# Optimization experiments

Hardware: AMD Instinct MI355X
Metric: run time of the kernel (lower is better)

Reference implementation:

```python
import jax, jax.numpy as jnp
import numpy as np

N = 20000      # nodes
E = 320000     # edges (before self-loops)
F_IN = 512     # input feature size
HID = 128      # encoder hidden
OUT = 128      # encoder output / GAT in_channels
H = 4          # gat heads
C = 64         # gat out_channels per head


def setup_inputs() -> dict:
    key = jax.random.key(0)
    ks = jax.random.split(key, 10)
    s = 0.05
    return {
        "x": jax.random.normal(ks[0], (N, F_IN), jnp.float32),
        "edge_index": jax.random.randint(ks[1], (2, E), 0, N, dtype=jnp.int64),
        "W1": jax.random.normal(ks[2], (F_IN, HID), jnp.float32) * s,
        "b1": jax.random.normal(ks[3], (HID,), jnp.float32) * s,
        "W2": jax.random.normal(ks[4], (HID, OUT), jnp.float32) * s,
        "b2": jax.random.normal(ks[5], (OUT,), jnp.float32) * s,
        "Wg": jax.random.normal(ks[6], (OUT, H * C), jnp.float32) * s,
        "att_src": jax.random.normal(ks[7], (H, C), jnp.float32) * s,
        "att_dst": jax.random.normal(ks[8], (H, C), jnp.float32) * s,
        "bias_g": jax.random.normal(ks[9], (H * C,), jnp.float32) * s,
    }


def reference(x, edge_index, W1, b1, W2, b2, Wg, att_src, att_dst, bias_g):
    # MLP encoder: Linear -> ReLU -> Linear
    h = jnp.maximum(x @ W1 + b1, 0.0) @ W2 + b2            # [N, OUT]

    # GATConv (concat=True, eval mode -> no dropout)
    xg = (h @ Wg).reshape(N, H, C)                          # per-head projections

    # add self-loops (PyG GATConv default)
    loops = jnp.arange(N, dtype=edge_index.dtype)
    src = jnp.concatenate([edge_index[0], loops])           # [E+N] source j
    dst = jnp.concatenate([edge_index[1], loops])           # [E+N] dest   i

    a_src = jnp.einsum('nhc,hc->nh', xg, att_src)           # [N, H]
    a_dst = jnp.einsum('nhc,hc->nh', xg, att_dst)           # [N, H]

    e = jax.nn.leaky_relu(a_src[src] + a_dst[dst], 0.2)     # [E+N, H]

    # segment softmax over incoming edges of each destination node
    m = jax.ops.segment_max(e, dst, num_segments=N)         # [N, H]
    ex = jnp.exp(e - m[dst])
    denom = jax.ops.segment_sum(ex, dst, num_segments=N)
    alpha = ex / (denom[dst] + 1e-16)                       # [E+N, H]

    # weighted scatter-add aggregation
    out = jax.ops.segment_sum(alpha[:, :, None] * xg[src], dst, num_segments=N)  # [N, H, C]
    return out.reshape(N, H * C) + bias_g
```

## Files before the change

### kernel.cpp

```cpp
#include <hip/hip_runtime.h>
#include <math.h>

#define NNODES 20000
#define NEDGES 320000
#define FIN    512
#define HIDD   128
#define OUTD   128
#define NH     4
#define NC     64
#define HC     256

typedef short bf16x8 __attribute__((ext_vector_type(8)));
typedef float f32x4  __attribute__((ext_vector_type(4)));

__device__ __forceinline__ unsigned short f2bf(float f) {
    unsigned int u = __float_as_uint(f);
    unsigned int r = 0x7fffu + ((u >> 16) & 1u);
    return (unsigned short)((u + r) >> 16);
}
__device__ __forceinline__ float b2f(short t) {
    return __uint_as_float(((unsigned)(unsigned short)t) << 16);
}
__device__ __forceinline__ float4 f4max(float4 a, float4 b) {
    return make_float4(fmaxf(a.x,b.x), fmaxf(a.y,b.y), fmaxf(a.z,b.z), fmaxf(a.w,b.w));
}
__device__ __forceinline__ float4 f4add(float4 a, float4 b) {
    return make_float4(a.x+b.x, a.y+b.y, a.z+b.z, a.w+b.w);
}
__device__ __forceinline__ float4 f4sub(float4 a, float4 b) {
    return make_float4(a.x-b.x, a.y-b.y, a.z-b.z, a.w-b.w);
}
__device__ __forceinline__ float4 f4mul(float4 a, float4 b) {
    return make_float4(a.x*b.x, a.y*b.y, a.z*b.z, a.w*b.w);
}
__device__ __forceinline__ float4 f4exp(float4 a) {
    return make_float4(__expf(a.x), __expf(a.y), __expf(a.z), __expf(a.w));
}
__device__ __forceinline__ float4 shflx4(float4 v, int m) {
    return make_float4(__shfl_xor(v.x,m), __shfl_xor(v.y,m), __shfl_xor(v.z,m), __shfl_xor(v.w,m));
}

__global__ __launch_bounds__(256)
void transpose_cast_kernel(const float* __restrict__ W, unsigned short* __restrict__ Wt,
                           int K, int N) {
    int idx = blockIdx.x * 256 + threadIdx.x;
    if (idx >= K * N) return;
    int n = idx / K, k = idx % K;
    Wt[idx] = f2bf(W[(size_t)k * N + n]);
}

__global__ __launch_bounds__(256)
void fuse_w2g_kernel(const float* __restrict__ W2, const float* __restrict__ b2,
                     const float* __restrict__ Wg, unsigned short* __restrict__ W2gt,
                     float* __restrict__ b2g) {
    int idx = blockIdx.x * 256 + threadIdx.x;
    if (idx >= HC * HIDD) return;
    int n = idx >> 7;
    int k = idx & 127;
    float s = 0.f;
    #pragma unroll 8
    for (int t = 0; t < HIDD; ++t)
        s += W2[(size_t)k * OUTD + t] * Wg[(size_t)t * HC + n];
    W2gt[(size_t)n * HIDD + k] = f2bf(s);
    if (k == 0) {
        float t2 = 0.f;
        #pragma unroll 8
        for (int t = 0; t < OUTD; ++t) t2 += b2[t] * Wg[(size_t)t * HC + n];
        b2g[n] = t2;
    }
}

template<bool A_IS_F32, bool OUT_BF16>
__global__ __launch_bounds__(256)
void mfma_gemm_kernel(const void* __restrict__ Aptr,
                      const unsigned short* __restrict__ Bt,
                      const float* __restrict__ bias,
                      void* __restrict__ Cptr,
                      int M, int N, int K, int do_relu) {
    __shared__ unsigned short As[64 * 64];
    __shared__ unsigned short Bs[128 * 64];

    const int tid  = threadIdx.x;
    const int lane = tid & 63;
    const int w    = tid >> 6;
    const int wr   = w >> 1;
    const int wc   = w & 1;
    const int m0   = blockIdx.x * 64;
    const int n0   = blockIdx.y * 128;

    char* pA = (char*)As;
    char* pB = (char*)Bs;

    f32x4 acc[2][4];
    #pragma unroll
    for (int m = 0; m < 2; ++m)
        #pragma unroll
        for (int n = 0; n < 4; ++n) acc[m][n] = (f32x4){0.f, 0.f, 0.f, 0.f};

    for (int k0 = 0; k0 < K; k0 += 64) {
        if (A_IS_F32) {
            const int row = tid >> 2;
            const int ks  = (tid & 3) << 4;
            const bool ok = (m0 + row) < M;
            const float4* Ap = (const float4*)((const float*)Aptr +
                               (size_t)(m0 + row) * K + k0 + ks);
            float4 f0 = make_float4(0,0,0,0), f1 = f0, f2 = f0, f3 = f0;
            if (ok) { f0 = Ap[0]; f1 = Ap[1]; f2 = Ap[2]; f3 = Ap[3]; }
            unsigned short u[16];
            u[0]=f2bf(f0.x); u[1]=f2bf(f0.y); u[2]=f2bf(f0.z); u[3]=f2bf(f0.w);
            u[4]=f2bf(f1.x); u[5]=f2bf(f1.y); u[6]=f2bf(f1.z); u[7]=f2bf(f1.w);
            u[8]=f2bf(f2.x); u[9]=f2bf(f2.y); u[10]=f2bf(f2.z); u[11]=f2bf(f2.w);
            u[12]=f2bf(f3.x); u[13]=f2bf(f3.y); u[14]=f2bf(f3.z); u[15]=f2bf(f3.w);
            const int sw = (row & 7) << 4;
            const int base = row * 128 + ks * 2;
            *(bf16x8*)(pA + ((base     ) ^ sw)) = *(bf16x8*)&u[0];
            *(bf16x8*)(pA + ((base + 16) ^ sw)) = *(bf16x8*)&u[8];
        } else {
            const unsigned short* Ab = (const unsigned short*)Aptr;
            #pragma unroll
            for (int i = 0; i < 2; ++i) {
                int s   = tid + i * 256;
                int row = s >> 3;
                int sg  = s & 7;
                bf16x8 v = {};
                if ((m0 + row) < M)
                    v = *(const bf16x8*)(Ab + (size_t)(m0 + row) * K + k0 + sg * 8);
                *(bf16x8*)(pA + (((row * 128 + sg * 16)) ^ ((row & 7) << 4))) = v;
            }
        }
        #pragma unroll
        for (int i = 0; i < 4; ++i) {
            int s   = tid + i * 256;
            int col = s >> 3;
            int sg  = s & 7;
            bf16x8 v = *(const bf16x8*)(Bt + (size_t)(n0 + col) * K + k0 + sg * 8);
            *(bf16x8*)(pB + (((col * 128 + sg * 16)) ^ ((col & 7) << 4))) = v;
        }
        __syncthreads();

        #pragma unroll
        for (int ks = 0; ks < 2; ++ks) {
            const int kb = ks * 64 + ((lane >> 4) << 4);
            bf16x8 a[2], b[4];
            #pragma unroll
            for (int m = 0; m < 2; ++m) {
                int row = wr * 32 + m * 16 + (lane & 15);
                a[m] = *(const bf16x8*)(pA + ((row * 128 + kb) ^ ((row & 7) << 4)));
            }
            #pragma unroll
            for (int n = 0; n < 4; ++n) {
                int col = wc * 64 + n * 16 + (lane & 15);
                b[n] = *(const bf16x8*)(pB + ((col * 128 + kb) ^ ((col & 7) << 4)));
            }
            #pragma unroll
            for (int m = 0; m < 2; ++m)
                #pragma unroll
                for (int n = 0; n < 4; ++n)
                    acc[m][n] = __builtin_amdgcn_mfma_f32_16x16x32_bf16(
                        a[m], b[n], acc[m][n], 0, 0, 0);
        }
        __syncthreads();
    }

    #pragma unroll
    for (int n = 0; n < 4; ++n) {
        const int col = n0 + wc * 64 + n * 16 + (lane & 15);
        const float bv = bias ? bias[col] : 0.f;
        #pragma unroll
        for (int m = 0; m < 2; ++m) {
            #pragma unroll
            for (int r = 0; r < 4; ++r) {
                const int row = m0 + wr * 32 + m * 16 + ((lane >> 4) << 2) + r;
                if (row >= M) continue;
                float v = acc[m][n][r] + bv;
                if (do_relu) v = fmaxf(v, 0.f);
                if (OUT_BF16)
                    ((unsigned short*)Cptr)[(size_t)row * N + col] = f2bf(v);
                else
                    ((float*)Cptr)[(size_t)row * N + col] = v;
            }
        }
    }
}

__global__ __launch_bounds__(256)
void att_dots_kernel(const unsigned short* __restrict__ xgb, const float* __restrict__ att_src,
                     const float* __restrict__ att_dst, float* __restrict__ a_src,
                     float* __restrict__ a_dst, int n) {
    int idx = blockIdx.x * 256 + threadIdx.x;
    if (idx >= n * NH) return;
    int node = idx >> 2;
    int h = idx & 3;
    const bf16x8* xr = (const bf16x8*)(xgb + (size_t)node * HC + h * NC);
    const float* sa = att_src + h * NC;
    const float* da = att_dst + h * NC;
    float ss = 0.f, dd = 0.f;
    #pragma unroll
    for (int j = 0; j < 8; ++j) {
        bf16x8 v = xr[j];
        #pragma unroll
        for (int t = 0; t < 8; ++t) {
            float f = b2f(v[t]);
            ss += f * sa[j * 8 + t];
            dd += f * da[j * 8 + t];
        }
    }
    a_src[idx] = ss;
    a_dst[idx] = dd;
}

__global__ void init_deg_kernel(int* __restrict__ deg, int n) {
    int i = blockIdx.x * 256 + threadIdx.x;
    if (i < n) deg[i] = 1;
}

__global__ void count_deg_kernel(const int* __restrict__ dst, int* __restrict__ deg, int e) {
    int i = blockIdx.x * 256 + threadIdx.x;
    if (i < e) atomicAdd(&deg[dst[i]], 1);
}

__global__ __launch_bounds__(1024)
void scan_offsets_kernel(const int* __restrict__ deg, int* __restrict__ offs,
                         int* __restrict__ cursor, int n) {
    __shared__ int wsum[16], wbase[16];
    const int tid = threadIdx.x, lane = tid & 63, w = tid >> 6;
    const int i0 = tid * 20;
    int loc[20];
    int s = 0;
    #pragma unroll
    for (int k = 0; k < 20; ++k) {
        int i = i0 + k;
        int v = (i < n) ? deg[i] : 0;
        loc[k] = s;
        s += v;
    }
    int incl = s;
    #pragma unroll
    for (int d = 1; d < 64; d <<= 1) {
        int t = __shfl_up(incl, d);
        if (lane >= d) incl += t;
    }
    if (lane == 63) wsum[w] = incl;
    __syncthreads();
    if (w == 0) {
        int v = (lane < 16) ? wsum[lane] : 0;
        int sc = v;
        #pragma unroll
        for (int d = 1; d < 16; d <<= 1) {
            int t = __shfl_up(sc, d);
            if (lane >= d) sc += t;
        }
        if (lane < 16) wbase[lane] = sc - v;
    }
    __syncthreads();
    const int excl = wbase[w] + incl - s;
    #pragma unroll
    for (int k = 0; k < 20; ++k) {
        int i = i0 + k;
        if (i < n) { int o = excl + loc[k]; offs[i] = o; cursor[i] = o; }
    }
    if (tid == 1023) offs[n] = excl + s;
}

__global__ void scatter_e_kernel(const int* __restrict__ src, const int* __restrict__ dst,
                                 const float4* __restrict__ asrc, const float4* __restrict__ adst,
                                 int* __restrict__ cursor, int* __restrict__ csr_src,
                                 float4* __restrict__ e_csr, int e, int n) {
    int i = blockIdx.x * 256 + threadIdx.x;
    int s, d;
    if (i < e)          { s = src[i]; d = dst[i]; }
    else if (i < e + n) { s = i - e;  d = i - e;  }
    else return;
    float4 a = asrc[s], b = adst[d];
    float4 ev = make_float4(a.x + b.x, a.y + b.y, a.z + b.z, a.w + b.w);
    ev.x = ev.x > 0.f ? ev.x : 0.2f * ev.x;
    ev.y = ev.y > 0.f ? ev.y : 0.2f * ev.y;
    ev.z = ev.z > 0.f ? ev.z : 0.2f * ev.z;
    ev.w = ev.w > 0.f ? ev.w : 0.2f * ev.w;
    int slot = atomicAdd(&cursor[d], 1);
    csr_src[slot] = s;
    e_csr[slot] = ev;
}

__global__ __launch_bounds__(256)
void gat_aggregate2_kernel(const unsigned short* __restrict__ xgb,
                           const float4* __restrict__ e_csr,
                           const int* __restrict__ offs, const int* __restrict__ csr_src,
                           const float* __restrict__ bias, float* __restrict__ out, int n) {
    __shared__ float4 exbuf[4][64];
    __shared__ int    sbuf[4][64];
    const int wv   = threadIdx.x >> 6;
    const int lane = threadIdx.x & 63;
    const int node = blockIdx.x * 4 + wv;
    if (node >= n) return;
    const int beg = offs[node], end = offs[node + 1];
    const int deg = end - beg;

    float4 m   = make_float4(-INFINITY, -INFINITY, -INFINITY, -INFINITY);
    float4 den = make_float4(0.f, 0.f, 0.f, 0.f);
    for (int c0 = 0; c0 < deg; c0 += 64) {
        int idx = beg + c0 + lane;
        bool ok = idx < end;
        float4 e = ok ? e_csr[idx]
                      : make_float4(-INFINITY, -INFINITY, -INFINITY, -INFINITY);
        int s = ok ? csr_src[idx] : 0;
        float4 cm = e;
        #pragma unroll
        for (int dd = 32; dd >= 1; dd >>= 1) cm = f4max(cm, shflx4(cm, dd));
        float4 nm = f4max(m, cm);
        float4 ex = f4exp(f4sub(e, nm));
        exbuf[wv][lane] = ex;
        sbuf[wv][lane]  = s;
        float4 cs = ex;
        #pragma unroll
        for (int dd = 32; dd >= 1; dd >>= 1) cs = f4add(cs, shflx4(cs, dd));
        den = f4add(f4mul(den, f4exp(f4sub(m, nm))), cs);
        m = nm;
    }

    const int hi = lane >> 5;
    const int ll = lane & 31;
    const int h  = ll >> 3;
    const float denh = (h == 0) ? den.x : (h == 1) ? den.y : (h == 2) ? den.z : den.w;
    const float inv = 1.f / (denh + 1e-16f);

    float4 acc0 = make_float4(0.f, 0.f, 0.f, 0.f);
    float4 acc1 = make_float4(0.f, 0.f, 0.f, 0.f);
    const float* exf = (const float*)&exbuf[wv][0];

    auto run_chunk = [&](int cn) {
        int j = 0;
        for (; j + 4 <= cn; j += 4) {
            int jA = j + hi, jB = j + 2 + hi;
            int sA = sbuf[wv][jA], sB = sbuf[wv][jB];
            float wA = exf[jA * 4 + h], wB = exf[jB * 4 + h];
            bf16x8 vA = *(const bf16x8*)(xgb + (size_t)sA * HC + ll * 8);
            bf16x8 vB = *(const bf16x8*)(xgb + (size_t)sB * HC + ll * 8);
            acc0.x += wA * b2f(vA[0]); acc0.y += wA * b2f(vA[1]);
            acc0.z += wA * b2f(vA[2]); acc0.w += wA * b2f(vA[3]);
            acc1.x += wA * b2f(vA[4]); acc1.y += wA * b2f(vA[5]);
            acc1.z += wA * b2f(vA[6]); acc1.w += wA * b2f(vA[7]);
            acc0.x += wB * b2f(vB[0]); acc0.y += wB * b2f(vB[1]);
            acc0.z += wB * b2f(vB[2]); acc0.w += wB * b2f(vB[3]);
            acc1.x += wB * b2f(vB[4]); acc1.y += wB * b2f(vB[5]);
            acc1.z += wB * b2f(vB[6]); acc1.w += wB * b2f(vB[7]);
        }
        for (; j < cn; j += 2) {
            int jj = j + hi;
            bool ok2 = jj < cn;
            int s = sbuf[wv][ok2 ? jj : 0];
            float wgt = ok2 ? exf[jj * 4 + h] : 0.f;
            bf16x8 v = *(const bf16x8*)(xgb + (size_t)s * HC + ll * 8);
            acc0.x += wgt * b2f(v[0]); acc0.y += wgt * b2f(v[1]);
            acc0.z += wgt * b2f(v[2]); acc0.w += wgt * b2f(v[3]);
            acc1.x += wgt * b2f(v[4]); acc1.y += wgt * b2f(v[5]);
            acc1.z += wgt * b2f(v[6]); acc1.w += wgt * b2f(v[7]);
        }
    };

    if (deg <= 64) {
        run_chunk(deg);
    } else {
        for (int c0 = 0; c0 < deg; c0 += 64) {
            int idx = beg + c0 + lane;
            if (idx < end) {
                float4 e = e_csr[idx];
                exbuf[wv][lane] = f4exp(f4sub(e, m));
                sbuf[wv][lane]  = csr_src[idx];
            }
            int cn = deg - c0; if (cn > 64) cn = 64;
            run_chunk(cn);
        }
    }

    acc0.x += __shfl_xor(acc0.x, 32); acc0.y += __shfl_xor(acc0.y, 32);
    acc0.z += __shfl_xor(acc0.z, 32); acc0.w += __shfl_xor(acc0.w, 32);
    acc1.x += __shfl_xor(acc1.x, 32); acc1.y += __shfl_xor(acc1.y, 32);
    acc1.z += __shfl_xor(acc1.z, 32); acc1.w += __shfl_xor(acc1.w, 32);

    if (hi == 0) {
        const float4* b4 = (const float4*)bias;
        float4 bv0 = b4[ll * 2], bv1 = b4[ll * 2 + 1];
        float4 o0 = make_float4(acc0.x * inv + bv0.x, acc0.y * inv + bv0.y,
                                acc0.z * inv + bv0.z, acc0.w * inv + bv0.w);
        float4 o1 = make_float4(acc1.x * inv + bv1.x, acc1.y * inv + bv1.y,
                                acc1.z * inv + bv1.z, acc1.w * inv + bv1.w);
        float4* op = (float4*)(out + (size_t)node * HC) + ll * 2;
        op[0] = o0;
        op[1] = o1;
    }
}

extern "C" void kernel_launch(void* const* d_in, const int* in_sizes, int n_in,
                              void* d_out, int out_size, void* d_ws, size_t ws_size,
                              hipStream_t stream) {
    const float* x       = (const float*)d_in[0];
    const int*   ei      = (const int*)d_in[1];
    const float* W1      = (const float*)d_in[2];
    const float* b1      = (const float*)d_in[3];
    const float* W2      = (const float*)d_in[4];
    const float* b2      = (const float*)d_in[5];
    const float* Wg      = (const float*)d_in[6];
    const float* att_src = (const float*)d_in[7];
    const float* att_dst = (const float*)d_in[8];
    const float* bias_g  = (const float*)d_in[9];

    const int Nn = in_sizes[0] / FIN;
    const int E  = in_sizes[1] / 2;
    const int* e_src = ei;
    const int* e_dst = ei + E;

    char* w = (char*)d_ws;
    auto alloc = [&](size_t bytes) { char* p = w; w += (bytes + 255) & ~(size_t)255; return p; };
    unsigned short* W1t  = (unsigned short*)alloc((size_t)OUTD * FIN * 2);
    unsigned short* W2gt = (unsigned short*)alloc((size_t)HC * HIDD * 2);
    float* b2g  = (float*)alloc(HC * 4);
    unsigned short* h1  = (unsigned short*)alloc((size_t)Nn * HIDD * 2);
    unsigned short* xgb = (unsigned short*)alloc((size_t)Nn * HC * 2);
    float* asrc = (float*)alloc((size_t)Nn * NH * 4);
    float* adst = (float*)alloc((size_t)Nn * NH * 4);
    int* deg    = (int*)alloc((size_t)Nn * 4);
    int* offs   = (int*)alloc((size_t)(Nn + 1) * 4);
    int* cursor = (int*)alloc((size_t)Nn * 4);
    int* csr    = (int*)alloc((size_t)(E + Nn) * 4);
    float4* ecsr = (float4*)alloc((size_t)(E + Nn) * 16);

    dim3 blk(256);
    const int gm = (Nn + 63) / 64;

    transpose_cast_kernel<<<dim3((FIN * HIDD + 255) / 256), blk, 0, stream>>>(W1, W1t, FIN, HIDD);
    fuse_w2g_kernel<<<dim3((HC * HIDD + 255) / 256), blk, 0, stream>>>(W2, b2, Wg, W2gt, b2g);

    mfma_gemm_kernel<true, true><<<dim3(gm, 1), blk, 0, stream>>>(
        x, W1t, b1, h1, Nn, HIDD, FIN, 1);
    mfma_gemm_kernel<false, true><<<dim3(gm, 2), blk, 0, stream>>>(
        h1, W2gt, b2g, xgb, Nn, HC, HIDD, 0);

    att_dots_kernel<<<dim3((Nn * NH + 255) / 256), blk, 0, stream>>>(
        xgb, att_src, att_dst, asrc, adst, Nn);

    init_deg_kernel<<<dim3((Nn + 255) / 256), blk, 0, stream>>>(deg, Nn);
    count_deg_kernel<<<dim3((E + 255) / 256), blk, 0, stream>>>(e_dst, deg, E);
    scan_offsets_kernel<<<dim3(1), dim3(1024), 0, stream>>>(deg, offs, cursor, Nn);
    scatter_e_kernel<<<dim3((E + Nn + 255) / 256), blk, 0, stream>>>(
        e_src, e_dst, (const float4*)asrc, (const float4*)adst, cursor, csr, ecsr, E, Nn);

    gat_aggregate2_kernel<<<dim3((Nn + 3) / 4), blk, 0, stream>>>(
        xgb, ecsr, offs, csr, bias_g, (float*)d_out, Nn);
}
```

Before: 153.7 us.

## Merge prep and count kernels, recompute edge scores in aggregation, retile first GEMM

Folds the weight transpose, W2·Wg fusion and degree init into one prep kernel, and merges the attention-dot and degree-count kernels into one launch. The scatter no longer writes a per-edge float4 score array; the aggregation kernel instead gathers a_src by source id and recomputes leaky-relu scores in both passes. The first GEMM uses a 32-row tile to launch more blocks, and the aggregation inner loop is unrolled to 4 gathers per half-wave with split output stores. This cuts launch count and edge-array memory traffic, at the cost of extra random gathers of a_src in the aggregation kernel.

```diff
diff --git a/kernel.cpp b/kernel.cpp
--- a/kernel.cpp
+++ b/kernel.cpp
@@ -41,43 +41,45 @@
 }
 
 __global__ __launch_bounds__(256)
-void transpose_cast_kernel(const float* __restrict__ W, unsigned short* __restrict__ Wt,
-                           int K, int N) {
+void prep_kernel(const float* __restrict__ W1, unsigned short* __restrict__ W1t,
+                 const float* __restrict__ W2, const float* __restrict__ b2,
+                 const float* __restrict__ Wg, unsigned short* __restrict__ W2gt,
+                 float* __restrict__ b2g, int* __restrict__ deg, int n) {
+    const int T1 = FIN * HIDD;
+    const int T2 = HC * HIDD;
     int idx = blockIdx.x * 256 + threadIdx.x;
-    if (idx >= K * N) return;
-    int n = idx / K, k = idx % K;
-    Wt[idx] = f2bf(W[(size_t)k * N + n]);
-}
-
-__global__ __launch_bounds__(256)
-void fuse_w2g_kernel(const float* __restrict__ W2, const float* __restrict__ b2,
-                     const float* __restrict__ Wg, unsigned short* __restrict__ W2gt,
-                     float* __restrict__ b2g) {
-    int idx = blockIdx.x * 256 + threadIdx.x;
-    if (idx >= HC * HIDD) return;
-    int n = idx >> 7;
-    int k = idx & 127;
-    float s = 0.f;
-    #pragma unroll 8
-    for (int t = 0; t < HIDD; ++t)
-        s += W2[(size_t)k * OUTD + t] * Wg[(size_t)t * HC + n];
-    W2gt[(size_t)n * HIDD + k] = f2bf(s);
-    if (k == 0) {
-        float t2 = 0.f;
+    if (idx < T1) {
+        int nn = idx / FIN, k = idx % FIN;
+        W1t[idx] = f2bf(W1[(size_t)k * HIDD + nn]);
+    } else if (idx < T1 + T2) {
+        int local = idx - T1;
+        int nn = local >> 7;
+        int k  = local & 127;
+        float s = 0.f;
         #pragma unroll 8
-        for (int t = 0; t < OUTD; ++t) t2 += b2[t] * Wg[(size_t)t * HC + n];
-        b2g[n] = t2;
-    }
-}
-
-template<bool A_IS_F32, bool OUT_BF16>
+        for (int t = 0; t < HIDD; ++t)
+            s += W2[(size_t)k * OUTD + t] * Wg[(size_t)t * HC + nn];
+        W2gt[(size_t)nn * HIDD + k] = f2bf(s);
+        if (k == 0) {
+            float t2 = 0.f;
+            #pragma unroll 8
+            for (int t = 0; t < OUTD; ++t) t2 += b2[t] * Wg[(size_t)t * HC + nn];
+            b2g[nn] = t2;
+        }
+    } else if (idx < T1 + T2 + n) {
+        deg[idx - T1 - T2] = 1;
+    }
+}
+
+template<bool A_IS_F32, bool OUT_BF16, int BM>
 __global__ __launch_bounds__(256)
 void mfma_gemm_kernel(const void* __restrict__ Aptr,
                       const unsigned short* __restrict__ Bt,
                       const float* __restrict__ bias,
                       void* __restrict__ Cptr,
                       int M, int N, int K, int do_relu) {
-    __shared__ unsigned short As[64 * 64];
+    constexpr int MF = BM / 32;
+    __shared__ unsigned short As[BM * 64];
     __shared__ unsigned short Bs[128 * 64];
 
     const int tid  = threadIdx.x;
@@ -85,40 +87,54 @@
     const int w    = tid >> 6;
     const int wr   = w >> 1;
     const int wc   = w & 1;
-    const int m0   = blockIdx.x * 64;
+    const int m0   = blockIdx.x * BM;
     const int n0   = blockIdx.y * 128;
 
     char* pA = (char*)As;
     char* pB = (char*)Bs;
 
-    f32x4 acc[2][4];
+    f32x4 acc[MF][4];
     #pragma unroll
-    for (int m = 0; m < 2; ++m)
+    for (int m = 0; m < MF; ++m)
         #pragma unroll
         for (int n = 0; n < 4; ++n) acc[m][n] = (f32x4){0.f, 0.f, 0.f, 0.f};
 
     for (int k0 = 0; k0 < K; k0 += 64) {
         if (A_IS_F32) {
-            const int row = tid >> 2;
-            const int ks  = (tid & 3) << 4;
-            const bool ok = (m0 + row) < M;
-            const float4* Ap = (const float4*)((const float*)Aptr +
-                               (size_t)(m0 + row) * K + k0 + ks);
-            float4 f0 = make_float4(0,0,0,0), f1 = f0, f2 = f0, f3 = f0;
-            if (ok) { f0 = Ap[0]; f1 = Ap[1]; f2 = Ap[2]; f3 = Ap[3]; }
-            unsigned short u[16];
-            u[0]=f2bf(f0.x); u[1]=f2bf(f0.y); u[2]=f2bf(f0.z); u[3]=f2bf(f0.w);
-            u[4]=f2bf(f1.x); u[5]=f2bf(f1.y); u[6]=f2bf(f1.z); u[7]=f2bf(f1.w);
-            u[8]=f2bf(f2.x); u[9]=f2bf(f2.y); u[10]=f2bf(f2.z); u[11]=f2bf(f2.w);
-            u[12]=f2bf(f3.x); u[13]=f2bf(f3.y); u[14]=f2bf(f3.z); u[15]=f2bf(f3.w);
-            const int sw = (row & 7) << 4;
-            const int base = row * 128 + ks * 2;
-            *(bf16x8*)(pA + ((base     ) ^ sw)) = *(bf16x8*)&u[0];
-            *(bf16x8*)(pA + ((base + 16) ^ sw)) = *(bf16x8*)&u[8];
+            if constexpr (BM == 64) {
+                const int row = tid >> 2;
+                const int ks  = (tid & 3) << 4;
+                const bool ok = (m0 + row) < M;
+                const float4* Ap = (const float4*)((const float*)Aptr +
+                                   (size_t)(m0 + row) * K + k0 + ks);
+                float4 f0 = make_float4(0,0,0,0), f1 = f0, f2 = f0, f3 = f0;
+                if (ok) { f0 = Ap[0]; f1 = Ap[1]; f2 = Ap[2]; f3 = Ap[3]; }
+                unsigned short u[16];
+                u[0]=f2bf(f0.x); u[1]=f2bf(f0.y); u[2]=f2bf(f0.z); u[3]=f2bf(f0.w);
+                u[4]=f2bf(f1.x); u[5]=f2bf(f1.y); u[6]=f2bf(f1.z); u[7]=f2bf(f1.w);
+                u[8]=f2bf(f2.x); u[9]=f2bf(f2.y); u[10]=f2bf(f2.z); u[11]=f2bf(f2.w);
+                u[12]=f2bf(f3.x); u[13]=f2bf(f3.y); u[14]=f2bf(f3.z); u[15]=f2bf(f3.w);
+                const int sw = (row & 7) << 4;
+                const int base = row * 128 + ks * 2;
+                *(bf16x8*)(pA + ((base     ) ^ sw)) = *(bf16x8*)&u[0];
+                *(bf16x8*)(pA + ((base + 16) ^ sw)) = *(bf16x8*)&u[8];
+            } else {
+                const int row = tid >> 3;
+                const int sg  = tid & 7;
+                const bool ok = (m0 + row) < M;
+                const float4* Ap = (const float4*)((const float*)Aptr +
+                                   (size_t)(m0 + row) * K + k0 + sg * 8);
+                float4 f0 = make_float4(0,0,0,0), f1 = f0;
+                if (ok) { f0 = Ap[0]; f1 = Ap[1]; }
+                unsigned short u[8];
+                u[0]=f2bf(f0.x); u[1]=f2bf(f0.y); u[2]=f2bf(f0.z); u[3]=f2bf(f0.w);
+                u[4]=f2bf(f1.x); u[5]=f2bf(f1.y); u[6]=f2bf(f1.z); u[7]=f2bf(f1.w);
+                *(bf16x8*)(pA + (((row * 128 + sg * 16)) ^ ((row & 7) << 4))) = *(bf16x8*)&u[0];
+            }
         } else {
             const unsigned short* Ab = (const unsigned short*)Aptr;
             #pragma unroll
-            for (int i = 0; i < 2; ++i) {
+            for (int i = 0; i < BM / 32; ++i) {
                 int s   = tid + i * 256;
                 int row = s >> 3;
                 int sg  = s & 7;
@@ -141,10 +157,10 @@
         #pragma unroll
         for (int ks = 0; ks < 2; ++ks) {
             const int kb = ks * 64 + ((lane >> 4) << 4);
-            bf16x8 a[2], b[4];
-            #pragma unroll
-            for (int m = 0; m < 2; ++m) {
-                int row = wr * 32 + m * 16 + (lane & 15);
+            bf16x8 a[MF], b[4];
+            #pragma unroll
+            for (int m = 0; m < MF; ++m) {
+                int row = wr * (16 * MF) + m * 16 + (lane & 15);
                 a[m] = *(const bf16x8*)(pA + ((row * 128 + kb) ^ ((row & 7) << 4)));
             }
             #pragma unroll
@@ -153,7 +169,7 @@
                 b[n] = *(const bf16x8*)(pB + ((col * 128 + kb) ^ ((col & 7) << 4)));
             }
             #pragma unroll
-            for (int m = 0; m < 2; ++m)
+            for (int m = 0; m < MF; ++m)
                 #pragma unroll
                 for (int n = 0; n < 4; ++n)
                     acc[m][n] = __builtin_amdgcn_mfma_f32_16x16x32_bf16(
@@ -167,10 +183,10 @@
         const int col = n0 + wc * 64 + n * 16 + (lane & 15);
         const float bv = bias ? bias[col] : 0.f;
         #pragma unroll
-        for (int m = 0; m < 2; ++m) {
+        for (int m = 0; m < MF; ++m) {
             #pragma unroll
             for (int r = 0; r < 4; ++r) {
-                const int row = m0 + wr * 32 + m * 16 + ((lane >> 4) << 2) + r;
+                const int row = m0 + wr * (16 * MF) + m * 16 + ((lane >> 4) << 2) + r;
                 if (row >= M) continue;
                 float v = acc[m][n][r] + bv;
                 if (do_relu) v = fmaxf(v, 0.f);
@@ -184,39 +200,36 @@
 }
 
 __global__ __launch_bounds__(256)
-void att_dots_kernel(const unsigned short* __restrict__ xgb, const float* __restrict__ att_src,
-                     const float* __restrict__ att_dst, float* __restrict__ a_src,
-                     float* __restrict__ a_dst, int n) {
-    int idx = blockIdx.x * 256 + threadIdx.x;
-    if (idx >= n * NH) return;
-    int node = idx >> 2;
-    int h = idx & 3;
-    const bf16x8* xr = (const bf16x8*)(xgb + (size_t)node * HC + h * NC);
-    const float* sa = att_src + h * NC;
-    const float* da = att_dst + h * NC;
-    float ss = 0.f, dd = 0.f;
-    #pragma unroll
-    for (int j = 0; j < 8; ++j) {
-        bf16x8 v = xr[j];
-        #pragma unroll
-        for (int t = 0; t < 8; ++t) {
-            float f = b2f(v[t]);
-            ss += f * sa[j * 8 + t];
-            dd += f * da[j * 8 + t];
-        }
-    }
-    a_src[idx] = ss;
-    a_dst[idx] = dd;
-}
-
-__global__ void init_deg_kernel(int* __restrict__ deg, int n) {
-    int i = blockIdx.x * 256 + threadIdx.x;
-    if (i < n) deg[i] = 1;
-}
-
-__global__ void count_deg_kernel(const int* __restrict__ dst, int* __restrict__ deg, int e) {
-    int i = blockIdx.x * 256 + threadIdx.x;
-    if (i < e) atomicAdd(&deg[dst[i]], 1);
+void dots_count_kernel(const unsigned short* __restrict__ xgb,
+                       const float* __restrict__ att_src, const float* __restrict__ att_dst,
+                       float* __restrict__ a_src, float* __restrict__ a_dst,
+                       const int* __restrict__ dst, int* __restrict__ deg,
+                       int n, int e, int nb_dots) {
+    if ((int)blockIdx.x < nb_dots) {
+        int idx = blockIdx.x * 256 + threadIdx.x;
+        if (idx >= n * NH) return;
+        int node = idx >> 2;
+        int h = idx & 3;
+        const bf16x8* xr = (const bf16x8*)(xgb + (size_t)node * HC + h * NC);
+        const float* sa = att_src + h * NC;
+        const float* da = att_dst + h * NC;
+        float ss = 0.f, dd = 0.f;
+        #pragma unroll
+        for (int j = 0; j < 8; ++j) {
+            bf16x8 v = xr[j];
+            #pragma unroll
+            for (int t = 0; t < 8; ++t) {
+                float f = b2f(v[t]);
+                ss += f * sa[j * 8 + t];
+                dd += f * da[j * 8 + t];
+            }
+        }
+        a_src[idx] = ss;
+        a_dst[idx] = dd;
+    } else {
+        int i = (blockIdx.x - nb_dots) * 256 + threadIdx.x;
+        if (i < e) atomicAdd(&deg[dst[i]], 1);
+    }
 }
 
 __global__ __launch_bounds__(1024)
@@ -262,29 +275,23 @@
     if (tid == 1023) offs[n] = excl + s;
 }
 
-__global__ void scatter_e_kernel(const int* __restrict__ src, const int* __restrict__ dst,
-                                 const float4* __restrict__ asrc, const float4* __restrict__ adst,
-                                 int* __restrict__ cursor, int* __restrict__ csr_src,
-                                 float4* __restrict__ e_csr, int e, int n) {
+__global__ void scatter_kernel(const int* __restrict__ src, const int* __restrict__ dst,
+                               int* __restrict__ cursor, int* __restrict__ csr_src,
+                               int e, int n) {
     int i = blockIdx.x * 256 + threadIdx.x;
-    int s, d;
-    if (i < e)          { s = src[i]; d = dst[i]; }
-    else if (i < e + n) { s = i - e;  d = i - e;  }
-    else return;
-    float4 a = asrc[s], b = adst[d];
-    float4 ev = make_float4(a.x + b.x, a.y + b.y, a.z + b.z, a.w + b.w);
-    ev.x = ev.x > 0.f ? ev.x : 0.2f * ev.x;
-    ev.y = ev.y > 0.f ? ev.y : 0.2f * ev.y;
-    ev.z = ev.z > 0.f ? ev.z : 0.2f * ev.z;
-    ev.w = ev.w > 0.f ? ev.w : 0.2f * ev.w;
-    int slot = atomicAdd(&cursor[d], 1);
-    csr_src[slot] = s;
-    e_csr[slot] = ev;
+    if (i < e) {
+        int s = src[i], d = dst[i];
+        csr_src[atomicAdd(&cursor[d], 1)] = s;
+    } else if (i < e + n) {
+        int node = i - e;
+        csr_src[atomicAdd(&cursor[node], 1)] = node;
+    }
 }
 
 __global__ __launch_bounds__(256)
-void gat_aggregate2_kernel(const unsigned short* __restrict__ xgb,
-                           const float4* __restrict__ e_csr,
+void gat_aggregate3_kernel(const unsigned short* __restrict__ xgb,
+                           const float4* __restrict__ asrc4,
+                           const float4* __restrict__ adst4,
                            const int* __restrict__ offs, const int* __restrict__ csr_src,
                            const float* __restrict__ bias, float* __restrict__ out, int n) {
     __shared__ float4 exbuf[4][64];
@@ -295,15 +302,23 @@
     if (node >= n) return;
     const int beg = offs[node], end = offs[node + 1];
     const int deg = end - beg;
+    const float4 adstv = adst4[node];
 
     float4 m   = make_float4(-INFINITY, -INFINITY, -INFINITY, -INFINITY);
     float4 den = make_float4(0.f, 0.f, 0.f, 0.f);
     for (int c0 = 0; c0 < deg; c0 += 64) {
         int idx = beg + c0 + lane;
         bool ok = idx < end;
-        float4 e = ok ? e_csr[idx]
-                      : make_float4(-INFINITY, -INFINITY, -INFINITY, -INFINITY);
         int s = ok ? csr_src[idx] : 0;
+        float4 e = make_float4(-INFINITY, -INFINITY, -INFINITY, -INFINITY);
+        if (ok) {
+            float4 a = asrc4[s];
+            e = f4add(a, adstv);
+            e.x = e.x > 0.f ? e.x : 0.2f * e.x;
+            e.y = e.y > 0.f ? e.y : 0.2f * e.y;
+            e.z = e.z > 0.f ? e.z : 0.2f * e.z;
+            e.w = e.w > 0.f ? e.w : 0.2f * e.w;
+        }
         float4 cm = e;
         #pragma unroll
         for (int dd = 32; dd >= 1; dd >>= 1) cm = f4max(cm, shflx4(cm, dd));
@@ -328,33 +343,42 @@
     float4 acc1 = make_float4(0.f, 0.f, 0.f, 0.f);
     const float* exf = (const float*)&exbuf[wv][0];
 
+    auto do_edge = [&](int jj) {
+        int s = sbuf[wv][jj];
+        float wgt = exf[jj * 4 + h];
+        bf16x8 v = *(const bf16x8*)(xgb + (size_t)s * HC + ll * 8);
+        acc0.x += wgt * b2f(v[0]); acc0.y += wgt * b2f(v[1]);
+        acc0.z += wgt * b2f(v[2]); acc0.w += wgt * b2f(v[3]);
+        acc1.x += wgt * b2f(v[4]); acc1.y += wgt * b2f(v[5]);
+        acc1.z += wgt * b2f(v[6]); acc1.w += wgt * b2f(v[7]);
+    };
+
     auto run_chunk = [&](int cn) {
         int j = 0;
+        for (; j + 8 <= cn; j += 8) {
+            int j0 = j + hi, j1 = j + 2 + hi, j2 = j + 4 + hi, j3 = j + 6 + hi;
+            int s0 = sbuf[wv][j0], s1 = sbuf[wv][j1], s2 = sbuf[wv][j2], s3 = sbuf[wv][j3];
+            float w0 = exf[j0*4+h], w1 = exf[j1*4+h], w2 = exf[j2*4+h], w3 = exf[j3*4+h];
+            bf16x8 v0 = *(const bf16x8*)(xgb + (size_t)s0 * HC + ll * 8);
+            bf16x8 v1 = *(const bf16x8*)(xgb + (size_t)s1 * HC + ll * 8);
+            bf16x8 v2 = *(const bf16x8*)(xgb + (size_t)s2 * HC + ll * 8);
+            bf16x8 v3 = *(const bf16x8*)(xgb + (size_t)s3 * HC + ll * 8);
+            acc0.x += w0*b2f(v0[0]); acc0.y += w0*b2f(v0[1]); acc0.z += w0*b2f(v0[2]); acc0.w += w0*b2f(v0[3]);
+            acc1.x += w0*b2f(v0[4]); acc1.y += w0*b2f(v0[5]); acc1.z += w0*b2f(v0[6]); acc1.w += w0*b2f(v0[7]);
+            acc0.x += w1*b2f(v1[0]); acc0.y += w1*b2f(v1[1]); acc0.z += w1*b2f(v1[2]); acc0.w += w1*b2f(v1[3]);
+            acc1.x += w1*b2f(v1[4]); acc1.y += w1*b2f(v1[5]); acc1.z += w1*b2f(v1[6]); acc1.w += w1*b2f(v1[7]);
+            acc0.x += w2*b2f(v2[0]); acc0.y += w2*b2f(v2[1]); acc0.z += w2*b2f(v2[2]); acc0.w += w2*b2f(v2[3]);
+            acc1.x += w2*b2f(v2[4]); acc1.y += w2*b2f(v2[5]); acc1.z += w2*b2f(v2[6]); acc1.w += w2*b2f(v2[7]);
+            acc0.x += w3*b2f(v3[0]); acc0.y += w3*b2f(v3[1]); acc0.z += w3*b2f(v3[2]); acc0.w += w3*b2f(v3[3]);
+            acc1.x += w3*b2f(v3[4]); acc1.y += w3*b2f(v3[5]); acc1.z += w3*b2f(v3[6]); acc1.w += w3*b2f(v3[7]);
+        }
         for (; j + 4 <= cn; j += 4) {
-            int jA = j + hi, jB = j + 2 + hi;
-            int sA = sbuf[wv][jA], sB = sbuf[wv][jB];
-            float wA = exf[jA * 4 + h], wB = exf[jB * 4 + h];
-            bf16x8 vA = *(const bf16x8*)(xgb + (size_t)sA * HC + ll * 8);
-            bf16x8 vB = *(const bf16x8*)(xgb + (size_t)sB * HC + ll * 8);
-            acc0.x += wA * b2f(vA[0]); acc0.y += wA * b2f(vA[1]);
-            acc0.z += wA * b2f(vA[2]); acc0.w += wA * b2f(vA[3]);
-            acc1.x += wA * b2f(vA[4]); acc1.y += wA * b2f(vA[5]);
-            acc1.z += wA * b2f(vA[6]); acc1.w += wA * b2f(vA[7]);
-            acc0.x += wB * b2f(vB[0]); acc0.y += wB * b2f(vB[1]);
-            acc0.z += wB * b2f(vB[2]); acc0.w += wB * b2f(vB[3]);
-            acc1.x += wB * b2f(vB[4]); acc1.y += wB * b2f(vB[5]);
-            acc1.z += wB * b2f(vB[6]); acc1.w += wB * b2f(vB[7]);
+            do_edge(j + hi);
+            do_edge(j + 2 + hi);
         }
         for (; j < cn; j += 2) {
             int jj = j + hi;
-            bool ok2 = jj < cn;
-            int s = sbuf[wv][ok2 ? jj : 0];
-            float wgt = ok2 ? exf[jj * 4 + h] : 0.f;
-            bf16x8 v = *(const bf16x8*)(xgb + (size_t)s * HC + ll * 8);
-            acc0.x += wgt * b2f(v[0]); acc0.y += wgt * b2f(v[1]);
-            acc0.z += wgt * b2f(v[2]); acc0.w += wgt * b2f(v[3]);
-            acc1.x += wgt * b2f(v[4]); acc1.y += wgt * b2f(v[5]);
-            acc1.z += wgt * b2f(v[6]); acc1.w += wgt * b2f(v[7]);
+            if (jj < cn) do_edge(jj);
         }
     };
 
@@ -364,9 +388,14 @@
         for (int c0 = 0; c0 < deg; c0 += 64) {
             int idx = beg + c0 + lane;
             if (idx < end) {
-                float4 e = e_csr[idx];
+                int s = csr_src[idx];
+                float4 e = f4add(asrc4[s], adstv);
+                e.x = e.x > 0.f ? e.x : 0.2f * e.x;
+                e.y = e.y > 0.f ? e.y : 0.2f * e.y;
+                e.z = e.z > 0.f ? e.z : 0.2f * e.z;
+                e.w = e.w > 0.f ? e.w : 0.2f * e.w;
                 exbuf[wv][lane] = f4exp(f4sub(e, m));
-                sbuf[wv][lane]  = csr_src[idx];
+                sbuf[wv][lane]  = s;
             }
             int cn = deg - c0; if (cn > 64) cn = 64;
             run_chunk(cn);
@@ -378,16 +407,16 @@
     acc1.x += __shfl_xor(acc1.x, 32); acc1.y += __shfl_xor(acc1.y, 32);
     acc1.z += __shfl_xor(acc1.z, 32); acc1.w += __shfl_xor(acc1.w, 32);
 
+    const float4* b4 = (const float4*)bias;
+    float4* op = (float4*)(out + (size_t)node * HC);
     if (hi == 0) {
-        const float4* b4 = (const float4*)bias;
-        float4 bv0 = b4[ll * 2], bv1 = b4[ll * 2 + 1];
-        float4 o0 = make_float4(acc0.x * inv + bv0.x, acc0.y * inv + bv0.y,
-                                acc0.z * inv + bv0.z, acc0.w * inv + bv0.w);
-        float4 o1 = make_float4(acc1.x * inv + bv1.x, acc1.y * inv + bv1.y,
-                                acc1.z * inv + bv1.z, acc1.w * inv + bv1.w);
-        float4* op = (float4*)(out + (size_t)node * HC) + ll * 2;
-        op[0] = o0;
-        op[1] = o1;
+        float4 bv = b4[ll * 2];
+        op[ll * 2] = make_float4(acc0.x * inv + bv.x, acc0.y * inv + bv.y,
+                                 acc0.z * inv + bv.z, acc0.w * inv + bv.w);
+    } else {
+        float4 bv = b4[ll * 2 + 1];
+        op[ll * 2 + 1] = make_float4(acc1.x * inv + bv.x, acc1.y * inv + bv.y,
+                                     acc1.z * inv + bv.z, acc1.w * inv + bv.w);
     }
 }
 
@@ -423,28 +452,32 @@
     int* offs   = (int*)alloc((size_t)(Nn + 1) * 4);
     int* cursor = (int*)alloc((size_t)Nn * 4);
     int* csr    = (int*)alloc((size_t)(E + Nn) * 4);
-    float4* ecsr = (float4*)alloc((size_t)(E + Nn) * 16);
 
     dim3 blk(256);
-    const int gm = (Nn + 63) / 64;
-
-    transpose_cast_kernel<<<dim3((FIN * HIDD + 255) / 256), blk, 0, stream>>>(W1, W1t, FIN, HIDD);
-    fuse_w2g_kernel<<<dim3((HC * HIDD + 255) / 256), blk, 0, stream>>>(W2, b2, Wg, W2gt, b2g);
-
-    mfma_gemm_kernel<true, true><<<dim3(gm, 1), blk, 0, stream>>>(
+
+    {
+        int total = FIN * HIDD + HC * HIDD + Nn;
+        prep_kernel<<<dim3((total + 255) / 256), blk, 0, stream>>>(
+            W1, W1t, W2, b2, Wg, W2gt, b2g, deg, Nn);
+    }
+
+    mfma_gemm_kernel<true, true, 32><<<dim3((Nn + 31) / 32, 1), blk, 0, stream>>>(
         x, W1t, b1, h1, Nn, HIDD, FIN, 1);
-    mfma_gemm_kernel<false, true><<<dim3(gm, 2), blk, 0, stream>>>(
+    mfma_gemm_kernel<false, true, 64><<<dim3((Nn + 63) / 64, 2), blk, 0, stream>>>(
         h1, W2gt, b2g, xgb, Nn, HC, HIDD, 0);
 
-    att_dots_kernel<<<dim3((Nn * NH + 255) / 256), blk, 0, stream>>>(
-        xgb, att_src, att_dst, asrc, adst, Nn);
-
-    init_deg_kernel<<<dim3((Nn + 255) / 256), blk, 0, stream>>>(deg, Nn);
-    count_deg_kernel<<<dim3((E + 255) / 256), blk, 0, stream>>>(e_dst, deg, E);
+    {
+        int nb_dots = (Nn * NH + 255) / 256;
+        int nb_cnt  = (E + 255) / 256;
+        dots_count_kernel<<<dim3(nb_dots + nb_cnt), blk, 0, stream>>>(
+            xgb, att_src, att_dst, asrc, adst, e_dst, deg, Nn, E, nb_dots);
+    }
+
     scan_offsets_kernel<<<dim3(1), dim3(1024), 0, stream>>>(deg, offs, cursor, Nn);
-    scatter_e_kernel<<<dim3((E + Nn + 255) / 256), blk, 0, stream>>>(
-        e_src, e_dst, (const float4*)asrc, (const float4*)adst, cursor, csr, ecsr, E, Nn);
-
-    gat_aggregate2_kernel<<<dim3((Nn + 3) / 4), blk, 0, stream>>>(
-        xgb, ecsr, offs, csr, bias_g, (float*)d_out, Nn);
-}
+    scatter_kernel<<<dim3((E + Nn + 255) / 256), blk, 0, stream>>>(
+        e_src, e_dst, cursor, csr, E, Nn);
+
+    gat_aggregate3_kernel<<<dim3((Nn + 3) / 4), blk, 0, stream>>>(
+        xgb, (const float4*)asrc, (const float4*)adst, offs, csr, bias_g,
+        (float*)d_out, Nn);
+}
```

New measurement: 130.1 us. -15.3%, faster.
